# Kernel tuning notes

Hardware: AMD Instinct MI355X
Metric: run time of the kernel (lower is better)

## Reference

```python
import jax, jax.numpy as jnp
import numpy as np

# ---- larq ste_sign: forward = sign (0 -> +1), backward = clipped straight-through ----
def _sign(x):
    return jnp.where(x >= 0, jnp.ones_like(x), -jnp.ones_like(x))

@jax.custom_vjp
def ste_sign(x):
    return _sign(x)

def _ste_fwd(x):
    return _sign(x), x

def _ste_bwd(x, g):
    return (g * (jnp.abs(x) <= 1.0).astype(g.dtype),)

ste_sign.defvjp(_ste_fwd, _ste_bwd)

BN_EPS = 1e-3  # keras BatchNormalization default epsilon

def conv2d(x, w, padding):
    # x: NHWC, w: HWIO
    return jax.lax.conv_general_dilated(
        x, w, window_strides=(1, 1), padding=padding,
        dimension_numbers=('NHWC', 'HWIO', 'NHWC'))

def maxpool2(x):
    return jax.lax.reduce_window(x, -jnp.inf, jax.lax.max,
                                 (1, 2, 2, 1), (1, 2, 2, 1), 'VALID')

def batchnorm(x, mean, var, beta):
    # BatchNormalization(scale=False): gamma fixed at 1
    return (x - mean) * jax.lax.rsqrt(var + BN_EPS) + beta


def setup_inputs() -> dict:
    key = jax.random.key(0)
    ks = jax.random.split(key, 20)
    d = {}
    d['x'] = jax.random.normal(ks[0], (64, 128, 128, 3), dtype=jnp.float32)
    d['w1'] = jax.random.normal(ks[1], (3, 3, 3, 32), dtype=jnp.float32)
    d['m1'] = jax.random.normal(ks[2], (32,), dtype=jnp.float32)
    d['v1'] = jax.random.uniform(ks[3], (32,), dtype=jnp.float32)
    d['b1'] = jax.random.normal(ks[4], (32,), dtype=jnp.float32)
    d['w2'] = jax.random.normal(ks[5], (3, 3, 32, 64), dtype=jnp.float32)
    d['m2'] = jax.random.normal(ks[6], (64,), dtype=jnp.float32)
    d['v2'] = jax.random.uniform(ks[7], (64,), dtype=jnp.float32)
    d['b2'] = jax.random.normal(ks[8], (64,), dtype=jnp.float32)
    d['w3'] = jax.random.normal(ks[9], (3, 3, 64, 128), dtype=jnp.float32)
    d['m3'] = jax.random.normal(ks[10], (128,), dtype=jnp.float32)
    d['v3'] = jax.random.uniform(ks[11], (128,), dtype=jnp.float32)
    d['b3'] = jax.random.normal(ks[12], (128,), dtype=jnp.float32)
    d['w4'] = jax.random.normal(ks[13], (3, 3, 128, 256), dtype=jnp.float32)
    d['m4'] = jax.random.normal(ks[14], (256,), dtype=jnp.float32)
    d['v4'] = jax.random.uniform(ks[15], (256,), dtype=jnp.float32)
    d['b4'] = jax.random.normal(ks[16], (256,), dtype=jnp.float32)
    return d


def reference(x, w1, m1, v1, b1, w2, m2, v2, b2, w3, m3, v3, b3, w4, m4, v4, b4):
    # Stem: QuantConv2D(32,3x3,valid) with kernel quantized only (no input quantizer)
    y = conv2d(x, ste_sign(w1), 'VALID')          # [B,126,126,32]
    y = batchnorm(maxpool2(y), m1, v1, b1)        # [B,63,63,32]
    # Three binarized blocks: ste_sign(input) conv ste_sign(kernel), same padding
    for w, m, v, b in ((w2, m2, v2, b2), (w3, m3, v3, b3), (w4, m4, v4, b4)):
        y = conv2d(ste_sign(y), ste_sign(w), 'SAME')
        y = batchnorm(maxpool2(y), m, v, b)       # halves spatial dims
    return y                                      # [B,7,7,256]
```

## Files before the change

### kernel.cpp

```cpp
#include <hip/hip_runtime.h>
#include <stdint.h>

#define BN_EPS 1e-3f

template <int CIN, int COUT>
__device__ inline void packw(const float* __restrict__ w, uint32_t* __restrict__ wp, int idx) {
    const int CINW = CIN / 32;
    int co = idx % COUT;
    int t2 = idx / COUT;
    int wi = t2 % CINW;
    int tap = t2 / CINW;
    uint32_t word = 0;
#pragma unroll
    for (int bb = 0; bb < 32; bb++) {
        float val = w[((tap * CIN) + wi * 32 + bb) * COUT + co];
        word |= (uint32_t)(val < 0.f) << bb;
    }
    wp[idx] = word;
}

__global__ void pack_all(const float* __restrict__ w1, const float* __restrict__ w2,
                         const float* __restrict__ w3, const float* __restrict__ w4,
                         uint32_t* __restrict__ w1m, uint32_t* __restrict__ w2p,
                         uint32_t* __restrict__ w3p, uint32_t* __restrict__ w4p) {
    int idx = blockIdx.x * 256 + threadIdx.x;
    if (idx < 27) {
        uint32_t word = 0;
#pragma unroll
        for (int c = 0; c < 32; c++)
            word |= (uint32_t)(w1[idx * 32 + c] < 0.f) << c;
        w1m[idx] = word;
        return;
    }
    idx -= 27;
    if (idx < 576) { packw<32, 64>(w2, w2p, idx); return; }
    idx -= 576;
    if (idx < 2304) { packw<64, 128>(w3, w3p, idx); return; }
    idx -= 2304;
    if (idx < 9216) { packw<128, 256>(w4, w4p, idx); return; }
}

__global__ __launch_bounds__(256) void conv1_k(const float* __restrict__ x,
                                               const uint32_t* __restrict__ w1m,
                                               const float* __restrict__ m1,
                                               const float* __restrict__ v1,
                                               const float* __restrict__ b1,
                                               uint32_t* __restrict__ y1p) {
    __shared__ float xt[34 * 104];

    int tile = blockIdx.x;
    int tx = tile & 3;
    int ty = (tile >> 2) & 3;
    int n  = tile >> 4;
    int ph0 = ty * 16, pw0 = tx * 16;
    int r0 = 2 * ph0;
    int cf0 = pw0 * 6;

    for (int i = threadIdx.x; i < 34 * 102; i += 256) {
        int r = i / 102, c = i % 102;
        int gr = r0 + r, gcf = cf0 + c;
        float vv = 0.f;
        if (gr < 128 && gcf < 384)
            vv = x[(size_t)(n * 128 + gr) * 384 + gcf];
        xt[r * 104 + c] = vv;
    }

    uint32_t um[27];
#pragma unroll
    for (int t = 0; t < 27; t++)
        um[t] = __builtin_amdgcn_readfirstlane(w1m[t]);

    __syncthreads();

    int wave = threadIdx.x >> 6, lane = threadIdx.x & 63;
    int px = lane & 15, py = (wave << 2) + (lane >> 4);
    int ph = ph0 + py, pw = pw0 + px;

    float win[48];
#pragma unroll
    for (int r = 0; r < 4; r++) {
        const float2* bp = (const float2*)&xt[(2 * py + r) * 104 + 6 * px];
#pragma unroll
        for (int q = 0; q < 6; q++) {
            float2 f2 = bp[q];
            win[r * 12 + 2 * q]     = f2.x;
            win[r * 12 + 2 * q + 1] = f2.y;
        }
    }

    uint32_t word = 0;
    for (int cg = 0; cg < 8; cg++) {
        float a[4][4];
#pragma unroll
        for (int j = 0; j < 4; j++)
#pragma unroll
            for (int p = 0; p < 4; p++) a[j][p] = 0.f;
#pragma unroll
        for (int kh = 0; kh < 3; kh++)
#pragma unroll
            for (int kw = 0; kw < 3; kw++)
#pragma unroll
                for (int ci = 0; ci < 3; ci++) {
                    int tap = (kh * 3 + kw) * 3 + ci;
                    float x00 = win[kh * 12 + kw * 3 + ci];
                    float x01 = win[kh * 12 + (kw + 1) * 3 + ci];
                    float x10 = win[(kh + 1) * 12 + kw * 3 + ci];
                    float x11 = win[(kh + 1) * 12 + (kw + 1) * 3 + ci];
                    uint32_t mw = um[tap];
#pragma unroll
                    for (int j = 0; j < 4; j++) {
                        float w = (mw & (1u << (cg * 4 + j))) ? -1.f : 1.f;
                        a[j][0] += x00 * w;
                        a[j][1] += x01 * w;
                        a[j][2] += x10 * w;
                        a[j][3] += x11 * w;
                    }
                }
#pragma unroll
        for (int j = 0; j < 4; j++) {
            float mx = fmaxf(fmaxf(a[j][0], a[j][1]), fmaxf(a[j][2], a[j][3]));
            int ch = cg * 4 + j;
            float y = (mx - m1[ch]) * rsqrtf(v1[ch] + BN_EPS) + b1[ch];
            word |= (uint32_t)(y < 0.f) << ch;
        }
    }

    if (ph < 63 && pw < 63)
        y1p[(n * 63 + ph) * 63 + pw] = word;
}

__global__ __launch_bounds__(256) void bconv2(const uint32_t* __restrict__ y1p,
                                              const uint32_t* __restrict__ w2p,
                                              const float* __restrict__ m,
                                              const float* __restrict__ v,
                                              const float* __restrict__ b,
                                              uint2* __restrict__ y2p) {
    int gw = __builtin_amdgcn_readfirstlane(blockIdx.x * 4 + (threadIdx.x >> 6));
    int lane = threadIdx.x & 63;
    int pwg = gw & 7;
    int t = gw >> 3;
    int ph = t % 31;
    int n = t / 31;

    uint32_t wq[9];
#pragma unroll
    for (int tap = 0; tap < 9; tap++) wq[tap] = w2p[tap * 64 + lane];
    float mm = m[lane], vv = v[lane], bb = b[lane];

    uint2 o0, o1, o2, o3;

    if (ph > 0 && pwg > 0) {
        int row0 = 2 * ph - 1, col0 = 8 * pwg - 1;
        uint32_t win[4][10];
#pragma unroll
        for (int r = 0; r < 4; r++)
#pragma unroll
            for (int c = 0; c < 10; c++)
                win[r][c] = y1p[(n * 63 + row0 + r) * 63 + min(col0 + c, 62)];

        uint2 res[4];
#pragma unroll
        for (int p = 0; p < 4; p++) {
            int a0 = 0, a1 = 0, a2 = 0, a3 = 0;
#pragma unroll
            for (int kh = 0; kh < 3; kh++)
#pragma unroll
                for (int kw = 0; kw < 3; kw++) {
                    uint32_t w = wq[kh * 3 + kw];
                    a0 += __popc(win[kh][2 * p + kw] ^ w);
                    a1 += __popc(win[kh][2 * p + kw + 1] ^ w);
                    a2 += __popc(win[kh + 1][2 * p + kw] ^ w);
                    a3 += __popc(win[kh + 1][2 * p + kw + 1] ^ w);
                }
            int mn = min(min(a0, a1), min(a2, a3));
            int best = 288 - 2 * mn;
            float y = ((float)best - mm) * rsqrtf(vv + BN_EPS) + bb;
            unsigned long long bal = __ballot(y < 0.f);
            res[p] = make_uint2((uint32_t)bal, (uint32_t)(bal >> 32));
        }
        o0 = res[0]; o1 = res[1]; o2 = res[2]; o3 = res[3];
    } else {
        uint2 res[4];
#pragma unroll
        for (int p = 0; p < 4; p++) {
            int pw = 4 * pwg + p;
            int best = -1000000;
            if (pw < 31) {
#pragma unroll
                for (int dy = 0; dy < 2; dy++)
#pragma unroll
                    for (int dx = 0; dx < 2; dx++) {
                        int oh = 2 * ph + dy, ow = 2 * pw + dx;
                        int acc = 0, K = 0;
                        for (int kh = 0; kh < 3; kh++) {
                            int ih = oh - 1 + kh;
                            if (ih < 0 || ih >= 63) continue;
                            for (int kw = 0; kw < 3; kw++) {
                                int iw = ow - 1 + kw;
                                if (iw < 0 || iw >= 63) continue;
                                acc += __popc(y1p[(n * 63 + ih) * 63 + iw] ^ wq[kh * 3 + kw]);
                                K += 32;
                            }
                        }
                        best = max(best, K - 2 * acc);
                    }
            }
            float y = ((float)best - mm) * rsqrtf(vv + BN_EPS) + bb;
            unsigned long long bal = __ballot(y < 0.f);
            res[p] = make_uint2((uint32_t)bal, (uint32_t)(bal >> 32));
        }
        o0 = res[0]; o1 = res[1]; o2 = res[2]; o3 = res[3];
    }

    uint2 rr = o0;
    if (lane == 1) rr = o1;
    if (lane == 2) rr = o2;
    if (lane == 3) rr = o3;
    int pws = 4 * pwg + lane;
    if (lane < 4 && pws < 31)
        y2p[(n * 31 + ph) * 31 + pws] = rr;
}

__global__ __launch_bounds__(256) void bconv3(const uint2* __restrict__ y2p,
                                              const uint32_t* __restrict__ w3p,
                                              const float* __restrict__ m,
                                              const float* __restrict__ v,
                                              const float* __restrict__ b,
                                              uint32_t* __restrict__ y3p) {
    int gw = __builtin_amdgcn_readfirstlane(blockIdx.x * 4 + (threadIdx.x >> 6));
    int lane = threadIdx.x & 63;
    int half = gw & 1;
    int t = gw >> 1;
    int pwg = t & 7;
    t >>= 3;
    int ph = t % 15;
    int n = t / 15;
    int co = half * 64 + lane;

    uint32_t wq0[9], wq1[9];
#pragma unroll
    for (int tap = 0; tap < 9; tap++) {
        wq0[tap] = w3p[(tap * 2 + 0) * 128 + co];
        wq1[tap] = w3p[(tap * 2 + 1) * 128 + co];
    }
    float mm = m[co], vv = v[co], bb = b[co];

    unsigned long long bal0, bal1;

    if (ph > 0 && pwg > 0) {
        int row0 = 2 * ph - 1, col0 = 4 * pwg - 1;
        uint2 win[4][6];
#pragma unroll
        for (int r = 0; r < 4; r++)
#pragma unroll
            for (int c = 0; c < 6; c++)
                win[r][c] = y2p[(n * 31 + row0 + r) * 31 + min(col0 + c, 30)];

        unsigned long long bals[2];
#pragma unroll
        for (int p = 0; p < 2; p++) {
            int a0 = 0, a1 = 0, a2 = 0, a3 = 0;
#pragma unroll
            for (int kh = 0; kh < 3; kh++)
#pragma unroll
                for (int kw = 0; kw < 3; kw++) {
                    int tap = kh * 3 + kw;
                    uint32_t u0 = wq0[tap], u1 = wq1[tap];
                    a0 += __popc(win[kh][2 * p + kw].x ^ u0) + __popc(win[kh][2 * p + kw].y ^ u1);
                    a1 += __popc(win[kh][2 * p + kw + 1].x ^ u0) + __popc(win[kh][2 * p + kw + 1].y ^ u1);
                    a2 += __popc(win[kh + 1][2 * p + kw].x ^ u0) + __popc(win[kh + 1][2 * p + kw].y ^ u1);
                    a3 += __popc(win[kh + 1][2 * p + kw + 1].x ^ u0) + __popc(win[kh + 1][2 * p + kw + 1].y ^ u1);
                }
            int mn = min(min(a0, a1), min(a2, a3));
            int best = 576 - 2 * mn;
            float y = ((float)best - mm) * rsqrtf(vv + BN_EPS) + bb;
            bals[p] = __ballot(y < 0.f);
        }
        bal0 = bals[0]; bal1 = bals[1];
    } else {
        unsigned long long bals[2];
#pragma unroll
        for (int p = 0; p < 2; p++) {
            int pw = 2 * pwg + p;
            int best = -1000000;
            if (pw < 15) {
#pragma unroll
                for (int dy = 0; dy < 2; dy++)
#pragma unroll
                    for (int dx = 0; dx < 2; dx++) {
                        int oh = 2 * ph + dy, ow = 2 * pw + dx;
                        int acc = 0, K = 0;
                        for (int kh = 0; kh < 3; kh++) {
                            int ih = oh - 1 + kh;
                            if (ih < 0 || ih >= 31) continue;
                            for (int kw = 0; kw < 3; kw++) {
                                int iw = ow - 1 + kw;
                                if (iw < 0 || iw >= 31) continue;
                                uint2 iv = y2p[(n * 31 + ih) * 31 + iw];
                                int tap = kh * 3 + kw;
                                acc += __popc(iv.x ^ wq0[tap]) + __popc(iv.y ^ wq1[tap]);
                                K += 64;
                            }
                        }
                        best = max(best, K - 2 * acc);
                    }
            }
            float y = ((float)best - mm) * rsqrtf(vv + BN_EPS) + bb;
            bals[p] = __ballot(y < 0.f);
        }
        bal0 = bals[0]; bal1 = bals[1];
    }

    uint32_t val = (uint32_t)bal0;
    if (lane == 1) val = (uint32_t)(bal0 >> 32);
    if (lane == 2) val = (uint32_t)bal1;
    if (lane == 3) val = (uint32_t)(bal1 >> 32);
    int p = lane >> 1;
    int pw = 2 * pwg + p;
    if (lane < 4 && pw < 15) {
        int pixel = (n * 15 + ph) * 15 + pw;
        y3p[pixel * 4 + half * 2 + (lane & 1)] = val;
    }
}

__global__ __launch_bounds__(256) void bconv4(const uint4* __restrict__ y3p,
                                              const uint32_t* __restrict__ w4p,
                                              const float* __restrict__ m,
                                              const float* __restrict__ v,
                                              const float* __restrict__ b,
                                              float* __restrict__ out) {
    int pixel = blockIdx.x;
    int lane = threadIdx.x & 63;
    int co = (threadIdx.x >> 6) * 64 + lane;
    int pw = pixel % 7;
    int t = pixel / 7;
    int ph = t % 7;
    int n = t / 7;

    uint4 wq[9];
#pragma unroll
    for (int tap = 0; tap < 9; tap++) {
        wq[tap].x = w4p[(tap * 4 + 0) * 256 + co];
        wq[tap].y = w4p[(tap * 4 + 1) * 256 + co];
        wq[tap].z = w4p[(tap * 4 + 2) * 256 + co];
        wq[tap].w = w4p[(tap * 4 + 3) * 256 + co];
    }

    int best;
    if (ph > 0 && pw > 0) {
        const uint4* p = y3p + (n * 15 + (2 * ph - 1)) * 15 + (2 * pw - 1);
        int a0 = 0, a1 = 0, a2 = 0, a3 = 0;
#pragma unroll
        for (int r = 0; r < 4; r++)
#pragma unroll
            for (int c = 0; c < 4; c++) {
                uint4 iv = p[r * 15 + c];
#pragma unroll
                for (int kh = 0; kh < 3; kh++) {
                    int dy = r - kh;
                    if (dy < 0 || dy > 1) continue;
#pragma unroll
                    for (int kw = 0; kw < 3; kw++) {
                        int dx = c - kw;
                        if (dx < 0 || dx > 1) continue;
                        int tap = kh * 3 + kw;
                        int pc = __popc(iv.x ^ wq[tap].x) + __popc(iv.y ^ wq[tap].y)
                               + __popc(iv.z ^ wq[tap].z) + __popc(iv.w ^ wq[tap].w);
                        if (dy == 0 && dx == 0) a0 += pc;
                        else if (dy == 0) a1 += pc;
                        else if (dx == 0) a2 += pc;
                        else a3 += pc;
                    }
                }
            }
        best = max(max(1152 - 2 * a0, 1152 - 2 * a1), max(1152 - 2 * a2, 1152 - 2 * a3));
    } else {
        best = -1000000;
#pragma unroll
        for (int dy = 0; dy < 2; dy++)
#pragma unroll
            for (int dx = 0; dx < 2; dx++) {
                int oh = 2 * ph + dy, ow = 2 * pw + dx;
                int acc = 0, K = 0;
                for (int kh = 0; kh < 3; kh++) {
                    int ih = oh - 1 + kh;
                    if (ih < 0 || ih >= 15) continue;
                    for (int kw = 0; kw < 3; kw++) {
                        int iw = ow - 1 + kw;
                        if (iw < 0 || iw >= 15) continue;
                        uint4 iv = y3p[(n * 15 + ih) * 15 + iw];
                        int tap = kh * 3 + kw;
                        acc += __popc(iv.x ^ wq[tap].x) + __popc(iv.y ^ wq[tap].y)
                             + __popc(iv.z ^ wq[tap].z) + __popc(iv.w ^ wq[tap].w);
                        K += 128;
                    }
                }
                best = max(best, K - 2 * acc);
            }
    }
    float y = ((float)best - m[co]) * rsqrtf(v[co] + BN_EPS) + b[co];
    out[pixel * 256 + co] = y;
}

extern "C" void kernel_launch(void* const* d_in, const int* in_sizes, int n_in,
                              void* d_out, int out_size, void* d_ws, size_t ws_size,
                              hipStream_t stream) {
    const float* x  = (const float*)d_in[0];
    const float* w1 = (const float*)d_in[1];
    const float* m1 = (const float*)d_in[2];
    const float* v1 = (const float*)d_in[3];
    const float* b1 = (const float*)d_in[4];
    const float* w2 = (const float*)d_in[5];
    const float* m2 = (const float*)d_in[6];
    const float* v2 = (const float*)d_in[7];
    const float* b2 = (const float*)d_in[8];
    const float* w3 = (const float*)d_in[9];
    const float* m3 = (const float*)d_in[10];
    const float* v3 = (const float*)d_in[11];
    const float* b3 = (const float*)d_in[12];
    const float* w4 = (const float*)d_in[13];
    const float* m4 = (const float*)d_in[14];
    const float* v4 = (const float*)d_in[15];
    const float* b4 = (const float*)d_in[16];
    float* out = (float*)d_out;

    char* ws = (char*)d_ws;
    size_t off = 0;
    auto take = [&](size_t bytes) -> char* {
        char* p = ws + off;
        off += (bytes + 255) & ~(size_t)255;
        return p;
    };
    uint32_t* y1p = (uint32_t*)take((size_t)64 * 63 * 63 * 4);
    uint2*    y2p = (uint2*)take((size_t)64 * 31 * 31 * 8);
    uint32_t* y3p = (uint32_t*)take((size_t)64 * 15 * 15 * 16);
    uint32_t* w1m = (uint32_t*)take(27 * 4);
    uint32_t* w2p = (uint32_t*)take(576 * 4);
    uint32_t* w3p = (uint32_t*)take(2304 * 4);
    uint32_t* w4p = (uint32_t*)take(9216 * 4);

    pack_all<<<(12123 + 255) / 256, 256, 0, stream>>>(w1, w2, w3, w4, w1m, w2p, w3p, w4p);

    conv1_k<<<64 * 16, 256, 0, stream>>>(x, w1m, m1, v1, b1, y1p);

    bconv2<<<(64 * 31 * 8) / 4, 256, 0, stream>>>(y1p, w2p, m2, v2, b2, y2p);

    bconv3<<<(64 * 15 * 8 * 2) / 4, 256, 0, stream>>>(y2p, w3p, m3, v3, b3, y3p);

    bconv4<<<64 * 7 * 7, 256, 0, stream>>>((const uint4*)y3p, w4p, m4, v4, b4, out);
}
```

Before: 170.8 us.

## Fuse all layers into one persistent cooperative kernel with grid syncs

Replaces the five separate launches with one cooperative persistent kernel that packs weights, then runs conv1, bconv2, bconv3 and bconv4 as grid-stride phases separated by grid.sync. Batchnorm is folded into per-channel thresholds computed once, and conv1 is restructured to compute all 32 channels per pre-pool pixel, with max-pool done through lane shuffles. This removes launch gaps and tail effects between layers, at the cost of grid-wide barriers and a grid sized by occupancy. The threshold compare also assumes BN is monotonic in the conv sum, which holds because there is no gamma and the scale is positive. The old kernels remain as a fallback if the cooperative launch fails.

Measured after the change: 533.6 us. 212% more time.

```diff
diff --git a/kernel.cpp b/kernel.cpp
--- a/kernel.cpp
+++ b/kernel.cpp
@@ -1,10 +1,18 @@
 #include <hip/hip_runtime.h>
+#include <hip/hip_cooperative_groups.h>
 #include <stdint.h>
+#include <math.h>
+
+namespace cg = cooperative_groups;
 
 #define BN_EPS 1e-3f
 
+__device__ __forceinline__ uint32_t rfl_u32(uint32_t v) {
+    return __builtin_amdgcn_readfirstlane(v);
+}
+
 template <int CIN, int COUT>
-__device__ inline void packw(const float* __restrict__ w, uint32_t* __restrict__ wp, int idx) {
+__device__ inline void packw_item(const float* __restrict__ w, uint32_t* __restrict__ wp, int idx) {
     const int CINW = CIN / 32;
     int co = idx % COUT;
     int t2 = idx / COUT;
@@ -19,10 +27,371 @@
     wp[idx] = word;
 }
 
-__global__ void pack_all(const float* __restrict__ w1, const float* __restrict__ w2,
-                         const float* __restrict__ w3, const float* __restrict__ w4,
-                         uint32_t* __restrict__ w1m, uint32_t* __restrict__ w2p,
-                         uint32_t* __restrict__ w3p, uint32_t* __restrict__ w4p) {
+__device__ inline float mk_thr(const float* m, const float* v, const float* b, int c) {
+    return (float)((double)m[c] - (double)b[c] * sqrt((double)v[c] + (double)BN_EPS));
+}
+
+__global__ __launch_bounds__(256, 4) void fused(
+    const float* __restrict__ x,  const float* __restrict__ w1,
+    const float* __restrict__ w2, const float* __restrict__ w3, const float* __restrict__ w4,
+    const float* __restrict__ m1, const float* __restrict__ v1, const float* __restrict__ b1,
+    const float* __restrict__ m2, const float* __restrict__ v2, const float* __restrict__ b2,
+    const float* __restrict__ m3, const float* __restrict__ v3, const float* __restrict__ b3,
+    const float* __restrict__ m4, const float* __restrict__ v4, const float* __restrict__ b4,
+    uint32_t* __restrict__ w1m, float* __restrict__ thr1,
+    uint32_t* __restrict__ w2p, float* __restrict__ thr2,
+    uint32_t* __restrict__ w3p, float* __restrict__ thr3,
+    uint32_t* __restrict__ w4p,
+    uint32_t* __restrict__ y1p, uint2* __restrict__ y2p,
+    uint32_t* __restrict__ y3p, float* __restrict__ out)
+{
+    cg::grid_group grid = cg::this_grid();
+    const int lane = threadIdx.x & 63;
+    const int wgid = rfl_u32((uint32_t)((blockIdx.x * 256 + threadIdx.x) >> 6));
+    const int nwaves = gridDim.x * 4;
+
+    for (int i = blockIdx.x * 256 + threadIdx.x; i < 12347; i += gridDim.x * 256) {
+        int j = i;
+        if (j < 27) {
+            uint32_t word = 0;
+#pragma unroll
+            for (int c = 0; c < 32; c++)
+                word |= (uint32_t)(w1[j * 32 + c] < 0.f) << c;
+            w1m[j] = word;
+        } else if ((j -= 27) < 32) {
+            thr1[j] = mk_thr(m1, v1, b1, j);
+        } else if ((j -= 32) < 576) {
+            packw_item<32, 64>(w2, w2p, j);
+        } else if ((j -= 576) < 64) {
+            thr2[j] = mk_thr(m2, v2, b2, j);
+        } else if ((j -= 64) < 2304) {
+            packw_item<64, 128>(w3, w3p, j);
+        } else if ((j -= 2304) < 128) {
+            thr3[j] = mk_thr(m3, v3, b3, j);
+        } else if ((j -= 128) < 9216) {
+            packw_item<128, 256>(w4, w4p, j);
+        }
+    }
+    grid.sync();
+
+    {
+        __shared__ float xt[18 * 56];
+
+        uint32_t um[27];
+#pragma unroll
+        for (int t = 0; t < 27; t++) um[t] = rfl_u32(w1m[t]);
+        float th[32];
+#pragma unroll
+        for (int c = 0; c < 32; c++)
+            th[c] = __uint_as_float(rfl_u32(((const uint32_t*)thr1)[c]));
+
+        int wave = threadIdx.x >> 6;
+        int r = lane >> 3, c8 = lane & 7;
+        int ly = (wave >> 1) * 8 + r;
+        int lx = (wave & 1) * 8 + c8;
+
+        for (int tile = blockIdx.x; tile < 4096; tile += gridDim.x) {
+            int n = tile >> 6, ty = (tile >> 3) & 7, tx = tile & 7;
+            int oy = ty * 16;
+            int oxf = tx * 48;
+            __syncthreads();
+            for (int i = threadIdx.x; i < 972; i += 256) {
+                int rr = i / 54, cc = i % 54;
+                int gr = oy + rr, gc = oxf + cc;
+                float vv = 0.f;
+                if (gr < 128 && gc < 384)
+                    vv = x[(size_t)(n * 128 + gr) * 384 + gc];
+                xt[rr * 56 + cc] = vv;
+            }
+            __syncthreads();
+
+            float win[27];
+#pragma unroll
+            for (int kh = 0; kh < 3; kh++)
+#pragma unroll
+                for (int kk = 0; kk < 9; kk++)
+                    win[kh * 9 + kk] = xt[(ly + kh) * 56 + lx * 3 + kk];
+
+            float acc[32];
+#pragma unroll
+            for (int ch = 0; ch < 32; ch++) acc[ch] = 0.f;
+#pragma unroll
+            for (int t = 0; t < 27; t++) {
+                uint32_t mw = um[t];
+                float xv = win[t];
+#pragma unroll
+                for (int ch = 0; ch < 32; ch++) {
+                    float w = (mw & (1u << ch)) ? -1.f : 1.f;
+                    acc[ch] += xv * w;
+                }
+            }
+#pragma unroll
+            for (int ch = 0; ch < 32; ch++) {
+                float a = fmaxf(acc[ch], __shfl_xor(acc[ch], 1, 64));
+                acc[ch] = fmaxf(a, __shfl_xor(a, 8, 64));
+            }
+            if (((r | c8) & 1) == 0) {
+                int ph = (oy + ly) >> 1;
+                int pw = (tx * 16 + lx) >> 1;
+                if (ph < 63 && pw < 63) {
+                    uint32_t word = 0;
+#pragma unroll
+                    for (int ch = 0; ch < 32; ch++)
+                        word |= (uint32_t)(acc[ch] < th[ch]) << ch;
+                    y1p[(n * 63 + ph) * 63 + pw] = word;
+                }
+            }
+        }
+    }
+    grid.sync();
+
+    {
+        uint32_t wq[9];
+#pragma unroll
+        for (int t = 0; t < 9; t++) wq[t] = w2p[t * 64 + lane];
+        float th = thr2[lane];
+
+        for (int item = wgid; item < 64 * 31 * 8; item += nwaves) {
+            int pwg = item & 7;
+            int t2 = item >> 3;
+            int ph = t2 % 31;
+            int n = t2 / 31;
+
+            uint2 res[4];
+            if (ph > 0 && pwg > 0) {
+                int row0 = 2 * ph - 1, col0 = 8 * pwg - 1;
+                uint32_t win[4][10];
+#pragma unroll
+                for (int rr = 0; rr < 4; rr++)
+#pragma unroll
+                    for (int cc = 0; cc < 10; cc++)
+                        win[rr][cc] = y1p[(n * 63 + row0 + rr) * 63 + min(col0 + cc, 62)];
+#pragma unroll
+                for (int p = 0; p < 4; p++) {
+                    int a0 = 0, a1 = 0, a2 = 0, a3 = 0;
+#pragma unroll
+                    for (int kh = 0; kh < 3; kh++)
+#pragma unroll
+                        for (int kw = 0; kw < 3; kw++) {
+                            uint32_t w = wq[kh * 3 + kw];
+                            a0 += __popc(win[kh][2 * p + kw] ^ w);
+                            a1 += __popc(win[kh][2 * p + kw + 1] ^ w);
+                            a2 += __popc(win[kh + 1][2 * p + kw] ^ w);
+                            a3 += __popc(win[kh + 1][2 * p + kw + 1] ^ w);
+                        }
+                    int best = 288 - 2 * min(min(a0, a1), min(a2, a3));
+                    unsigned long long bal = __ballot((float)best < th);
+                    res[p] = make_uint2((uint32_t)bal, (uint32_t)(bal >> 32));
+                }
+            } else {
+#pragma unroll
+                for (int p = 0; p < 4; p++) {
+                    int pw = 4 * pwg + p;
+                    int best = -1000000;
+                    if (pw < 31) {
+#pragma unroll
+                        for (int dy = 0; dy < 2; dy++)
+#pragma unroll
+                            for (int dx = 0; dx < 2; dx++) {
+                                int oh = 2 * ph + dy, ow = 2 * pw + dx;
+                                int acc = 0, K = 0;
+                                for (int kh = 0; kh < 3; kh++) {
+                                    int ih = oh - 1 + kh;
+                                    if (ih < 0 || ih >= 63) continue;
+                                    for (int kw = 0; kw < 3; kw++) {
+                                        int iw = ow - 1 + kw;
+                                        if (iw < 0 || iw >= 63) continue;
+                                        acc += __popc(y1p[(n * 63 + ih) * 63 + iw] ^ wq[kh * 3 + kw]);
+                                        K += 32;
+                                    }
+                                }
+                                best = max(best, K - 2 * acc);
+                            }
+                    }
+                    unsigned long long bal = __ballot((float)best < th);
+                    res[p] = make_uint2((uint32_t)bal, (uint32_t)(bal >> 32));
+                }
+            }
+            uint2 rr = res[0];
+            if (lane == 1) rr = res[1];
+            if (lane == 2) rr = res[2];
+            if (lane == 3) rr = res[3];
+            int pws = 4 * pwg + lane;
+            if (lane < 4 && pws < 31)
+                y2p[(n * 31 + ph) * 31 + pws] = rr;
+        }
+    }
+    grid.sync();
+
+    {
+        int half = wgid & 1;
+        int co = half * 64 + lane;
+        uint32_t wq0[9], wq1[9];
+#pragma unroll
+        for (int t = 0; t < 9; t++) {
+            wq0[t] = w3p[(t * 2 + 0) * 128 + co];
+            wq1[t] = w3p[(t * 2 + 1) * 128 + co];
+        }
+        float th = thr3[co];
+
+        for (int it = (wgid >> 1); it < 64 * 15 * 8; it += (nwaves >> 1)) {
+            int pwg = it & 7;
+            int t2 = it >> 3;
+            int ph = t2 % 15;
+            int n = t2 / 15;
+
+            unsigned long long bals[2];
+            if (ph > 0 && pwg > 0) {
+                int row0 = 2 * ph - 1, col0 = 4 * pwg - 1;
+                uint2 win[4][6];
+#pragma unroll
+                for (int rr = 0; rr < 4; rr++)
+#pragma unroll
+                    for (int cc = 0; cc < 6; cc++)
+                        win[rr][cc] = y2p[(n * 31 + row0 + rr) * 31 + min(col0 + cc, 30)];
+#pragma unroll
+                for (int p = 0; p < 2; p++) {
+                    int a0 = 0, a1 = 0, a2 = 0, a3 = 0;
+#pragma unroll
+                    for (int kh = 0; kh < 3; kh++)
+#pragma unroll
+                        for (int kw = 0; kw < 3; kw++) {
+                            int tap = kh * 3 + kw;
+                            uint32_t u0 = wq0[tap], u1 = wq1[tap];
+                            a0 += __popc(win[kh][2 * p + kw].x ^ u0) + __popc(win[kh][2 * p + kw].y ^ u1);
+                            a1 += __popc(win[kh][2 * p + kw + 1].x ^ u0) + __popc(win[kh][2 * p + kw + 1].y ^ u1);
+                            a2 += __popc(win[kh + 1][2 * p + kw].x ^ u0) + __popc(win[kh + 1][2 * p + kw].y ^ u1);
+                            a3 += __popc(win[kh + 1][2 * p + kw + 1].x ^ u0) + __popc(win[kh + 1][2 * p + kw + 1].y ^ u1);
+                        }
+                    int best = 576 - 2 * min(min(a0, a1), min(a2, a3));
+                    bals[p] = __ballot((float)best < th);
+                }
+            } else {
+#pragma unroll
+                for (int p = 0; p < 2; p++) {
+                    int pw = 2 * pwg + p;
+                    int best = -1000000;
+                    if (pw < 15) {
+#pragma unroll
+                        for (int dy = 0; dy < 2; dy++)
+#pragma unroll
+                            for (int dx = 0; dx < 2; dx++) {
+                                int oh = 2 * ph + dy, ow = 2 * pw + dx;
+                                int acc = 0, K = 0;
+                                for (int kh = 0; kh < 3; kh++) {
+                                    int ih = oh - 1 + kh;
+                                    if (ih < 0 || ih >= 31) continue;
+                                    for (int kw = 0; kw < 3; kw++) {
+                                        int iw = ow - 1 + kw;
+                                        if (iw < 0 || iw >= 31) continue;
+                                        uint2 iv = y2p[(n * 31 + ih) * 31 + iw];
+                                        int tap = kh * 3 + kw;
+                                        acc += __popc(iv.x ^ wq0[tap]) + __popc(iv.y ^ wq1[tap]);
+                                        K += 64;
+                                    }
+                                }
+                                best = max(best, K - 2 * acc);
+                            }
+                    }
+                    bals[p] = __ballot((float)best < th);
+                }
+            }
+            uint32_t val = (uint32_t)bals[0];
+            if (lane == 1) val = (uint32_t)(bals[0] >> 32);
+            if (lane == 2) val = (uint32_t)bals[1];
+            if (lane == 3) val = (uint32_t)(bals[1] >> 32);
+            int p = lane >> 1;
+            int pw = 2 * pwg + p;
+            if (lane < 4 && pw < 15) {
+                int pixel = (n * 15 + ph) * 15 + pw;
+                y3p[pixel * 4 + half * 2 + (lane & 1)] = val;
+            }
+        }
+    }
+    grid.sync();
+
+    {
+        const uint4* y3q = (const uint4*)y3p;
+        int q = wgid & 3;
+        int co = q * 64 + lane;
+        uint4 wq[9];
+#pragma unroll
+        for (int t = 0; t < 9; t++) {
+            wq[t].x = w4p[(t * 4 + 0) * 256 + co];
+            wq[t].y = w4p[(t * 4 + 1) * 256 + co];
+            wq[t].z = w4p[(t * 4 + 2) * 256 + co];
+            wq[t].w = w4p[(t * 4 + 3) * 256 + co];
+        }
+        float mm = m4[co], vv = v4[co], bb = b4[co];
+
+        for (int pix = (wgid >> 2); pix < 3136; pix += (nwaves >> 2)) {
+            int pw = pix % 7;
+            int t2 = pix / 7;
+            int ph = t2 % 7;
+            int n = t2 / 7;
+
+            int best;
+            if (ph > 0 && pw > 0) {
+                const uint4* p = y3q + (n * 15 + (2 * ph - 1)) * 15 + (2 * pw - 1);
+                int a0 = 0, a1 = 0, a2 = 0, a3 = 0;
+#pragma unroll
+                for (int rr = 0; rr < 4; rr++)
+#pragma unroll
+                    for (int cc = 0; cc < 4; cc++) {
+                        uint4 iv = p[rr * 15 + cc];
+#pragma unroll
+                        for (int kh = 0; kh < 3; kh++) {
+                            int dy = rr - kh;
+                            if (dy < 0 || dy > 1) continue;
+#pragma unroll
+                            for (int kw = 0; kw < 3; kw++) {
+                                int dx = cc - kw;
+                                if (dx < 0 || dx > 1) continue;
+                                int tap = kh * 3 + kw;
+                                int pc = __popc(iv.x ^ wq[tap].x) + __popc(iv.y ^ wq[tap].y)
+                                       + __popc(iv.z ^ wq[tap].z) + __popc(iv.w ^ wq[tap].w);
+                                if (dy == 0 && dx == 0) a0 += pc;
+                                else if (dy == 0) a1 += pc;
+                                else if (dx == 0) a2 += pc;
+                                else a3 += pc;
+                            }
+                        }
+                    }
+                best = 1152 - 2 * min(min(a0, a1), min(a2, a3));
+            } else {
+                best = -1000000;
+#pragma unroll
+                for (int dy = 0; dy < 2; dy++)
+#pragma unroll
+                    for (int dx = 0; dx < 2; dx++) {
+                        int oh = 2 * ph + dy, ow = 2 * pw + dx;
+                        int acc = 0, K = 0;
+                        for (int kh = 0; kh < 3; kh++) {
+                            int ih = oh - 1 + kh;
+                            if (ih < 0 || ih >= 15) continue;
+                            for (int kw = 0; kw < 3; kw++) {
+                                int iw = ow - 1 + kw;
+                                if (iw < 0 || iw >= 15) continue;
+                                uint4 iv = y3q[(n * 15 + ih) * 15 + iw];
+                                int tap = kh * 3 + kw;
+                                acc += __popc(iv.x ^ wq[tap].x) + __popc(iv.y ^ wq[tap].y)
+                                     + __popc(iv.z ^ wq[tap].z) + __popc(iv.w ^ wq[tap].w);
+                                K += 128;
+                            }
+                        }
+                        best = max(best, K - 2 * acc);
+                    }
+            }
+            float y = ((float)best - mm) * rsqrtf(vv + BN_EPS) + bb;
+            out[pix * 256 + co] = y;
+        }
+    }
+}
+
+__global__ void fb_pack_all(const float* __restrict__ w1, const float* __restrict__ w2,
+                            const float* __restrict__ w3, const float* __restrict__ w4,
+                            uint32_t* __restrict__ w1m, uint32_t* __restrict__ w2p,
+                            uint32_t* __restrict__ w3p, uint32_t* __restrict__ w4p) {
     int idx = blockIdx.x * 256 + threadIdx.x;
     if (idx < 27) {
         uint32_t word = 0;
@@ -33,21 +402,20 @@
         return;
     }
     idx -= 27;
-    if (idx < 576) { packw<32, 64>(w2, w2p, idx); return; }
+    if (idx < 576) { packw_item<32, 64>(w2, w2p, idx); return; }
     idx -= 576;
-    if (idx < 2304) { packw<64, 128>(w3, w3p, idx); return; }
+    if (idx < 2304) { packw_item<64, 128>(w3, w3p, idx); return; }
     idx -= 2304;
-    if (idx < 9216) { packw<128, 256>(w4, w4p, idx); return; }
-}
-
-__global__ __launch_bounds__(256) void conv1_k(const float* __restrict__ x,
-                                               const uint32_t* __restrict__ w1m,
-                                               const float* __restrict__ m1,
-                                               const float* __restrict__ v1,
-                                               const float* __restrict__ b1,
-                                               uint32_t* __restrict__ y1p) {
+    if (idx < 9216) { packw_item<128, 256>(w4, w4p, idx); return; }
+}
+
+__global__ __launch_bounds__(256) void fb_conv1(const float* __restrict__ x,
+                                                const uint32_t* __restrict__ w1m,
+                                                const float* __restrict__ m1,
+                                                const float* __restrict__ v1,
+                                                const float* __restrict__ b1,
+                                                uint32_t* __restrict__ y1p) {
     __shared__ float xt[34 * 104];
-
     int tile = blockIdx.x;
     int tx = tile & 3;
     int ty = (tile >> 2) & 3;
@@ -64,12 +432,10 @@
             vv = x[(size_t)(n * 128 + gr) * 384 + gcf];
         xt[r * 104 + c] = vv;
     }
-
     uint32_t um[27];
 #pragma unroll
     for (int t = 0; t < 27; t++)
         um[t] = __builtin_amdgcn_readfirstlane(w1m[t]);
-
     __syncthreads();
 
     int wave = threadIdx.x >> 6, lane = threadIdx.x & 63;
@@ -87,9 +453,8 @@
             win[r * 12 + 2 * q + 1] = f2.y;
         }
     }
-
     uint32_t word = 0;
-    for (int cg = 0; cg < 8; cg++) {
+    for (int cg2 = 0; cg2 < 8; cg2++) {
         float a[4][4];
 #pragma unroll
         for (int j = 0; j < 4; j++)
@@ -109,7 +474,7 @@
                     uint32_t mw = um[tap];
 #pragma unroll
                     for (int j = 0; j < 4; j++) {
-                        float w = (mw & (1u << (cg * 4 + j))) ? -1.f : 1.f;
+                        float w = (mw & (1u << (cg2 * 4 + j))) ? -1.f : 1.f;
                         a[j][0] += x00 * w;
                         a[j][1] += x01 * w;
                         a[j][2] += x10 * w;
@@ -119,22 +484,21 @@
 #pragma unroll
         for (int j = 0; j < 4; j++) {
             float mx = fmaxf(fmaxf(a[j][0], a[j][1]), fmaxf(a[j][2], a[j][3]));
-            int ch = cg * 4 + j;
+            int ch = cg2 * 4 + j;
             float y = (mx - m1[ch]) * rsqrtf(v1[ch] + BN_EPS) + b1[ch];
             word |= (uint32_t)(y < 0.f) << ch;
         }
     }
-
     if (ph < 63 && pw < 63)
         y1p[(n * 63 + ph) * 63 + pw] = word;
 }
 
-__global__ __launch_bounds__(256) void bconv2(const uint32_t* __restrict__ y1p,
-                                              const uint32_t* __restrict__ w2p,
-                                              const float* __restrict__ m,
-                                              const float* __restrict__ v,
-                                              const float* __restrict__ b,
-                                              uint2* __restrict__ y2p) {
+__global__ __launch_bounds__(256) void fb_bconv2(const uint32_t* __restrict__ y1p,
+                                                 const uint32_t* __restrict__ w2p,
+                                                 const float* __restrict__ m,
+                                                 const float* __restrict__ v,
+                                                 const float* __restrict__ b,
+                                                 uint2* __restrict__ y2p) {
     int gw = __builtin_amdgcn_readfirstlane(blockIdx.x * 4 + (threadIdx.x >> 6));
     int lane = threadIdx.x & 63;
     int pwg = gw & 7;
@@ -147,8 +511,7 @@
     for (int tap = 0; tap < 9; tap++) wq[tap] = w2p[tap * 64 + lane];
     float mm = m[lane], vv = v[lane], bb = b[lane];
 
-    uint2 o0, o1, o2, o3;
-
+    uint2 res[4];
     if (ph > 0 && pwg > 0) {
         int row0 = 2 * ph - 1, col0 = 8 * pwg - 1;
         uint32_t win[4][10];
@@ -157,8 +520,6 @@
 #pragma unroll
             for (int c = 0; c < 10; c++)
                 win[r][c] = y1p[(n * 63 + row0 + r) * 63 + min(col0 + c, 62)];
-
-        uint2 res[4];
 #pragma unroll
         for (int p = 0; p < 4; p++) {
             int a0 = 0, a1 = 0, a2 = 0, a3 = 0;
@@ -172,15 +533,12 @@
                     a2 += __popc(win[kh + 1][2 * p + kw] ^ w);
                     a3 += __popc(win[kh + 1][2 * p + kw + 1] ^ w);
                 }
-            int mn = min(min(a0, a1), min(a2, a3));
-            int best = 288 - 2 * mn;
+            int best = 288 - 2 * min(min(a0, a1), min(a2, a3));
             float y = ((float)best - mm) * rsqrtf(vv + BN_EPS) + bb;
             unsigned long long bal = __ballot(y < 0.f);
             res[p] = make_uint2((uint32_t)bal, (uint32_t)(bal >> 32));
         }
-        o0 = res[0]; o1 = res[1]; o2 = res[2]; o3 = res[3];
     } else {
-        uint2 res[4];
 #pragma unroll
         for (int p = 0; p < 4; p++) {
             int pw = 4 * pwg + p;
@@ -209,24 +567,22 @@
             unsigned long long bal = __ballot(y < 0.f);
             res[p] = make_uint2((uint32_t)bal, (uint32_t)(bal >> 32));
         }
-        o0 = res[0]; o1 = res[1]; o2 = res[2]; o3 = res[3];
-    }
-
-    uint2 rr = o0;
-    if (lane == 1) rr = o1;
-    if (lane == 2) rr = o2;
-    if (lane == 3) rr = o3;
+    }
+    uint2 rr = res[0];
+    if (lane == 1) rr = res[1];
+    if (lane == 2) rr = res[2];
+    if (lane == 3) rr = res[3];
     int pws = 4 * pwg + lane;
     if (lane < 4 && pws < 31)
         y2p[(n * 31 + ph) * 31 + pws] = rr;
 }
 
-__global__ __launch_bounds__(256) void bconv3(const uint2* __restrict__ y2p,
-                                              const uint32_t* __restrict__ w3p,
-                                              const float* __restrict__ m,
-                                              const float* __restrict__ v,
-                                              const float* __restrict__ b,
-                                              uint32_t* __restrict__ y3p) {
+__global__ __launch_bounds__(256) void fb_bconv3(const uint2* __restrict__ y2p,
+                                                 const uint32_t* __restrict__ w3p,
+                                                 const float* __restrict__ m,
+                                                 const float* __restrict__ v,
+                                                 const float* __restrict__ b,
+                                                 uint32_t* __restrict__ y3p) {
     int gw = __builtin_amdgcn_readfirstlane(blockIdx.x * 4 + (threadIdx.x >> 6));
     int lane = threadIdx.x & 63;
     int half = gw & 1;
@@ -245,8 +601,7 @@
     }
     float mm = m[co], vv = v[co], bb = b[co];
 
-    unsigned long long bal0, bal1;
-
+    unsigned long long bals[2];
     if (ph > 0 && pwg > 0) {
         int row0 = 2 * ph - 1, col0 = 4 * pwg - 1;
         uint2 win[4][6];
@@ -255,8 +610,6 @@
 #pragma unroll
             for (int c = 0; c < 6; c++)
                 win[r][c] = y2p[(n * 31 + row0 + r) * 31 + min(col0 + c, 30)];
-
-        unsigned long long bals[2];
 #pragma unroll
         for (int p = 0; p < 2; p++) {
             int a0 = 0, a1 = 0, a2 = 0, a3 = 0;
@@ -271,14 +624,11 @@
                     a2 += __popc(win[kh + 1][2 * p + kw].x ^ u0) + __popc(win[kh + 1][2 * p + kw].y ^ u1);
                     a3 += __popc(win[kh + 1][2 * p + kw + 1].x ^ u0) + __popc(win[kh + 1][2 * p + kw + 1].y ^ u1);
                 }
-            int mn = min(min(a0, a1), min(a2, a3));
-            int best = 576 - 2 * mn;
+            int best = 576 - 2 * min(min(a0, a1), min(a2, a3));
             float y = ((float)best - mm) * rsqrtf(vv + BN_EPS) + bb;
             bals[p] = __ballot(y < 0.f);
         }
-        bal0 = bals[0]; bal1 = bals[1];
     } else {
-        unsigned long long bals[2];
 #pragma unroll
         for (int p = 0; p < 2; p++) {
             int pw = 2 * pwg + p;
@@ -308,13 +658,11 @@
             float y = ((float)best - mm) * rsqrtf(vv + BN_EPS) + bb;
             bals[p] = __ballot(y < 0.f);
         }
-        bal0 = bals[0]; bal1 = bals[1];
-    }
-
-    uint32_t val = (uint32_t)bal0;
-    if (lane == 1) val = (uint32_t)(bal0 >> 32);
-    if (lane == 2) val = (uint32_t)bal1;
-    if (lane == 3) val = (uint32_t)(bal1 >> 32);
+    }
+    uint32_t val = (uint32_t)bals[0];
+    if (lane == 1) val = (uint32_t)(bals[0] >> 32);
+    if (lane == 2) val = (uint32_t)bals[1];
+    if (lane == 3) val = (uint32_t)(bals[1] >> 32);
     int p = lane >> 1;
     int pw = 2 * pwg + p;
     if (lane < 4 && pw < 15) {
@@ -323,12 +671,12 @@
     }
 }
 
-__global__ __launch_bounds__(256) void bconv4(const uint4* __restrict__ y3p,
-                                              const uint32_t* __restrict__ w4p,
-                                              const float* __restrict__ m,
-                                              const float* __restrict__ v,
-                                              const float* __restrict__ b,
-                                              float* __restrict__ out) {
+__global__ __launch_bounds__(256) void fb_bconv4(const uint4* __restrict__ y3p,
+                                                 const uint32_t* __restrict__ w4p,
+                                                 const float* __restrict__ m,
+                                                 const float* __restrict__ v,
+                                                 const float* __restrict__ b,
+                                                 float* __restrict__ out) {
     int pixel = blockIdx.x;
     int lane = threadIdx.x & 63;
     int co = (threadIdx.x >> 6) * 64 + lane;
@@ -345,23 +693,22 @@
         wq[tap].z = w4p[(tap * 4 + 2) * 256 + co];
         wq[tap].w = w4p[(tap * 4 + 3) * 256 + co];
     }
-
     int best;
     if (ph > 0 && pw > 0) {
         const uint4* p = y3p + (n * 15 + (2 * ph - 1)) * 15 + (2 * pw - 1);
         int a0 = 0, a1 = 0, a2 = 0, a3 = 0;
 #pragma unroll
-        for (int r = 0; r < 4; r++)
-#pragma unroll
-            for (int c = 0; c < 4; c++) {
-                uint4 iv = p[r * 15 + c];
+        for (int rr = 0; rr < 4; rr++)
+#pragma unroll
+            for (int cc = 0; cc < 4; cc++) {
+                uint4 iv = p[rr * 15 + cc];
 #pragma unroll
                 for (int kh = 0; kh < 3; kh++) {
-                    int dy = r - kh;
+                    int dy = rr - kh;
                     if (dy < 0 || dy > 1) continue;
 #pragma unroll
                     for (int kw = 0; kw < 3; kw++) {
-                        int dx = c - kw;
+                        int dx = cc - kw;
                         if (dx < 0 || dx > 1) continue;
                         int tap = kh * 3 + kw;
                         int pc = __popc(iv.x ^ wq[tap].x) + __popc(iv.y ^ wq[tap].y)
@@ -373,7 +720,7 @@
                     }
                 }
             }
-        best = max(max(1152 - 2 * a0, 1152 - 2 * a1), max(1152 - 2 * a2, 1152 - 2 * a3));
+        best = 1152 - 2 * min(min(a0, a1), min(a2, a3));
     } else {
         best = -1000000;
 #pragma unroll
@@ -422,7 +769,7 @@
     const float* m4 = (const float*)d_in[14];
     const float* v4 = (const float*)d_in[15];
     const float* b4 = (const float*)d_in[16];
-    float* out = (float*)d_out;
+    float* outp = (float*)d_out;
 
     char* ws = (char*)d_ws;
     size_t off = 0;
@@ -431,21 +778,40 @@
         off += (bytes + 255) & ~(size_t)255;
         return p;
     };
-    uint32_t* y1p = (uint32_t*)take((size_t)64 * 63 * 63 * 4);
-    uint2*    y2p = (uint2*)take((size_t)64 * 31 * 31 * 8);
-    uint32_t* y3p = (uint32_t*)take((size_t)64 * 15 * 15 * 16);
-    uint32_t* w1m = (uint32_t*)take(27 * 4);
-    uint32_t* w2p = (uint32_t*)take(576 * 4);
-    uint32_t* w3p = (uint32_t*)take(2304 * 4);
-    uint32_t* w4p = (uint32_t*)take(9216 * 4);
-
-    pack_all<<<(12123 + 255) / 256, 256, 0, stream>>>(w1, w2, w3, w4, w1m, w2p, w3p, w4p);
-
-    conv1_k<<<64 * 16, 256, 0, stream>>>(x, w1m, m1, v1, b1, y1p);
-
-    bconv2<<<(64 * 31 * 8) / 4, 256, 0, stream>>>(y1p, w2p, m2, v2, b2, y2p);
-
-    bconv3<<<(64 * 15 * 8 * 2) / 4, 256, 0, stream>>>(y2p, w3p, m3, v3, b3, y3p);
-
-    bconv4<<<64 * 7 * 7, 256, 0, stream>>>((const uint4*)y3p, w4p, m4, v4, b4, out);
-}
+    uint32_t* y1p  = (uint32_t*)take((size_t)64 * 63 * 63 * 4);
+    uint2*    y2p  = (uint2*)take((size_t)64 * 31 * 31 * 8);
+    uint32_t* y3p  = (uint32_t*)take((size_t)64 * 15 * 15 * 16);
+    uint32_t* w1m  = (uint32_t*)take(27 * 4);
+    float*    thr1 = (float*)take(32 * 4);
+    uint32_t* w2p  = (uint32_t*)take(576 * 4);
+    float*    thr2 = (float*)take(64 * 4);
+    uint32_t* w3p  = (uint32_t*)take(2304 * 4);
+    float*    thr3 = (float*)take(128 * 4);
+    uint32_t* w4p  = (uint32_t*)take(9216 * 4);
+
+    int maxb = 0;
+    hipError_t oe = hipOccupancyMaxActiveBlocksPerMultiprocessor(&maxb, fused, 256, 0);
+    if (oe != hipSuccess || maxb < 1) maxb = 1;
+    int nblk = maxb * 256;
+    if (nblk > 4096) nblk = 4096;
+
+    void* args[] = {
+        (void*)&x,  (void*)&w1, (void*)&w2, (void*)&w3, (void*)&w4,
+        (void*)&m1, (void*)&v1, (void*)&b1,
+        (void*)&m2, (void*)&v2, (void*)&b2,
+        (void*)&m3, (void*)&v3, (void*)&b3,
+        (void*)&m4, (void*)&v4, (void*)&b4,
+        (void*)&w1m, (void*)&thr1, (void*)&w2p, (void*)&thr2,
+        (void*)&w3p, (void*)&thr3, (void*)&w4p,
+        (void*)&y1p, (void*)&y2p, (void*)&y3p, (void*)&outp
+    };
+    hipError_t le = hipLaunchCooperativeKernel((const void*)fused, dim3(nblk), dim3(256),
+                                               args, 0, stream);
+    if (le != hipSuccess) {
+        fb_pack_all<<<(12123 + 255) / 256, 256, 0, stream>>>(w1, w2, w3, w4, w1m, w2p, w3p, w4p);
+        fb_conv1<<<64 * 16, 256, 0, stream>>>(x, w1m, m1, v1, b1, y1p);
+        fb_bconv2<<<(64 * 31 * 8) / 4, 256, 0, stream>>>(y1p, w2p, m2, v2, b2, y2p);
+        fb_bconv3<<<(64 * 15 * 8 * 2) / 4, 256, 0, stream>>>(y2p, w3p, m3, v3, b3, y3p);
+        fb_bconv4<<<64 * 7 * 7, 256, 0, stream>>>((const uint4*)y3p, w4p, m4, v4, b4, outp);
+    }
+}
```
